# Performance work log

Hardware: AMD Instinct MI355X
Metric: run time of the kernel (lower is better)

The kernel has to match this reference:

```python
import jax, jax.numpy as jnp
import numpy as np

CLAMP_MIN, CLAMP_MAX = 1e-7, 10.0


def _hyper_layer(H, edge_nodes, W, b, power):
    """One HyperTensorGraphConvolution forward.

    H:          [N, d] node signals
    edge_nodes: [E, k] int node indices per hyperedge (k-1 < num_sample, so
                the sampling branch of the original code never triggers and the
                aggregation is the full power-mean over the k-1 neighbors)
    """
    H = jnp.clip(H, CLAMP_MIN, CLAMP_MAX)          # torch.clamp_(H, ...)
    inv_p = 1.0 / power
    Hp = H ** power                                 # [N, d]
    gathered = Hp[edge_nodes]                       # [E, k, d]
    edge_sum = gathered.sum(axis=1, keepdims=True)  # [E, 1, d]
    k = edge_nodes.shape[1]
    # power-mean of the other (k-1) nodes in the hyperedge, per incidence
    contrib = ((edge_sum - gathered) / (k - 1)) ** inv_p   # [E, k, d]
    # new_signal = H.clone(); scatter-add contributions per (edge, node)
    d = H.shape[1]
    new_signal = H.at[edge_nodes.reshape(-1)].add(contrib.reshape(-1, d))
    # row-normalize (rowsum^-1, inf -> 0)
    rowsum = new_signal.sum(axis=1, keepdims=True)
    r_inv = jnp.where(rowsum != 0, 1.0 / rowsum, 0.0)
    AH = new_signal * r_inv
    return AH @ W + b


def setup_inputs() -> dict:
    key = jax.random.key(0)
    k_x, k_e, k_w1, k_b1, k_w2, k_b2 = jax.random.split(key, 6)
    N, d, E, k, c = 100000, 128, 25000, 32, 40
    x = jax.random.uniform(k_x, (N, d), dtype=jnp.float32)
    edge_nodes = jax.random.randint(k_e, (E, k), 0, N, dtype=jnp.int64)
    std1 = 1.0 / np.sqrt(16.0)
    W1 = jax.random.uniform(k_w1, (d, 16), jnp.float32, -std1, std1)
    b1 = jax.random.uniform(k_b1, (16,), jnp.float32, -std1, std1)
    std2 = 1.0 / np.sqrt(float(c))
    W2 = jax.random.uniform(k_w2, (16, c), jnp.float32, -std2, std2)
    b2 = jax.random.uniform(k_b2, (c,), jnp.float32, -std2, std2)
    return {"x": x, "edge_nodes": edge_nodes, "W1": W1, "b1": b1,
            "W2": W2, "b2": b2, "power": 2}


def reference(x, edge_nodes, W1, b1, W2, b2, power):
    H = jax.nn.relu(_hyper_layer(x, edge_nodes, W1, b1, float(power)))
    # dropout is identity at inference
    out = _hyper_layer(H, edge_nodes, W2, b2, float(power))
    return out
```

## Files before the change

### kernel.cpp

```cpp
#include <hip/hip_runtime.h>
#include <hip/hip_fp16.h>
#include <math.h>

#define CAP 64
#define D1 128
#define D2 16
#define C_OUT 40
#define K_EDGE 32
#define CLAMP_LO 1e-7f
#define CLAMP_HI 10.0f
#define SQRT_INV31 0.1796053020267749f

typedef unsigned short ushort_t;

__global__ __launch_bounds__(256) void k_setup(const float* __restrict__ x,
                                               __half2* __restrict__ Hp,
                                               const int* __restrict__ idx,
                                               int* __restrict__ deg,
                                               ushort_t* __restrict__ lst,
                                               const float* __restrict__ W1,
                                               float* __restrict__ W1t,
                                               __half2* __restrict__ S,
                                               float* __restrict__ S2,
                                               int n4, int total, int E) {
    int i = blockIdx.x * 256 + threadIdx.x;
    if (i < n4) {
        float4 v = ((const float4*)x)[i];
        v.x = fminf(fmaxf(v.x, CLAMP_LO), CLAMP_HI);
        v.y = fminf(fmaxf(v.y, CLAMP_LO), CLAMP_HI);
        v.z = fminf(fmaxf(v.z, CLAMP_LO), CLAMP_HI);
        v.w = fminf(fmaxf(v.w, CLAMP_LO), CLAMP_HI);
        Hp[2 * i]     = __floats2half2_rn(v.x * v.x, v.y * v.y);
        Hp[2 * i + 1] = __floats2half2_rn(v.z * v.z, v.w * v.w);
    }
    if (i < total) {
        int n = idx[i];
        int e = i >> 5;
        int pos = atomicAdd(&deg[n], 1);
        if (pos < CAP) lst[n * CAP + pos] = (ushort_t)e;
    }
    if (i < D1 * D2) W1t[(i & 15) * D1 + (i >> 4)] = W1[i];
    if (i < 64) S[(size_t)E * 64 + i] = __floats2half2_rn(0.0f, 0.0f);
    if (i < D2) S2[(size_t)E * D2 + i] = 0.0f;
}

__global__ __launch_bounds__(256) void k_edge_sum(const __half2* __restrict__ Hp,
                                                  const int* __restrict__ idx,
                                                  __half2* __restrict__ S, int E) {
    int w = threadIdx.x >> 6;
    int lane = threadIdx.x & 63;
    int eA = blockIdx.x * 8 + w * 2;
    int nid = idx[eA * K_EDGE + lane];
    float a0 = 0.0f, a1 = 0.0f, b0 = 0.0f, b1 = 0.0f;
#pragma unroll
    for (int j = 0; j < K_EDGE; j++) {
        int nA = __builtin_amdgcn_readlane(nid, j);
        int nB = __builtin_amdgcn_readlane(nid, 32 + j);
        __half2 hA = Hp[(size_t)nA * 64 + lane];
        __half2 hB = Hp[(size_t)nB * 64 + lane];
        a0 += __low2float(hA); a1 += __high2float(hA);
        b0 += __low2float(hB); b1 += __high2float(hB);
    }
    S[(size_t)eA * 64 + lane]       = __floats2half2_rn(a0, a1);
    S[(size_t)(eA + 1) * 64 + lane] = __floats2half2_rn(b0, b1);
}

__global__ __launch_bounds__(256) void k_node1(const __half2* __restrict__ Hp,
                                               const __half2* __restrict__ S,
                                               const int* __restrict__ deg,
                                               const ushort_t* __restrict__ lst,
                                               const float* __restrict__ W1t,
                                               const float* __restrict__ b1,
                                               float* __restrict__ Hp2, int N, int E) {
    int w = threadIdx.x >> 6;
    int lane = threadIdx.x & 63;
    int pair = blockIdx.x * 4 + w;
    int n0 = pair * 2, n1 = n0 + 1;
    int c = lane & 15, j = lane >> 4;

    int2 dg2 = ((const int2*)deg)[pair];
    int dg0 = min(dg2.x, CAP), dg1 = min(dg2.y, CAP);
    int sl = lane & 15;
    int nodesel = (lane < 16) ? n0 : n1;
    ushort_t idu = (lane < 32) ? lst[nodesel * CAP + sl] : (ushort_t)0;
    int dsel = (lane < 16) ? dg0 : dg1;
    int e_sel = (lane < 32 && sl < dsel) ? (int)idu : E;

    __half2 hph0 = Hp[(size_t)n0 * 64 + lane];
    __half2 hph1 = Hp[(size_t)n1 * 64 + lane];

    __half2 sv0[16], sv1[16];
#pragma unroll
    for (int t = 0; t < 16; t++) {
        int e = __builtin_amdgcn_readlane(e_sel, t);
        sv0[t] = S[(size_t)e * 64 + lane];
    }
#pragma unroll
    for (int t = 0; t < 16; t++) {
        int e = __builtin_amdgcn_readlane(e_sel, 16 + t);
        sv1[t] = S[(size_t)e * 64 + lane];
    }

    float hp00 = __low2float(hph0), hp01 = __high2float(hph0);
    float hp10 = __low2float(hph1), hp11 = __high2float(hph1);

    float a00 = 0.0f, a01 = 0.0f, a10 = 0.0f, a11 = 0.0f;
#pragma unroll
    for (int t = 0; t < 16; t++) {
        a00 += __builtin_amdgcn_sqrtf(fmaxf(__low2float(sv0[t])  - hp00, 0.0f));
        a01 += __builtin_amdgcn_sqrtf(fmaxf(__high2float(sv0[t]) - hp01, 0.0f));
    }
#pragma unroll
    for (int t = 0; t < 16; t++) {
        a10 += __builtin_amdgcn_sqrtf(fmaxf(__low2float(sv1[t])  - hp10, 0.0f));
        a11 += __builtin_amdgcn_sqrtf(fmaxf(__high2float(sv1[t]) - hp11, 0.0f));
    }
    for (int t = 16; t < dg0; t++) {
        int e = lst[n0 * CAP + t];
        __half2 sh = S[(size_t)e * 64 + lane];
        a00 += __builtin_amdgcn_sqrtf(fmaxf(__low2float(sh)  - hp00, 0.0f));
        a01 += __builtin_amdgcn_sqrtf(fmaxf(__high2float(sh) - hp01, 0.0f));
    }
    for (int t = 16; t < dg1; t++) {
        int e = lst[n1 * CAP + t];
        __half2 sh = S[(size_t)e * 64 + lane];
        a10 += __builtin_amdgcn_sqrtf(fmaxf(__low2float(sh)  - hp10, 0.0f));
        a11 += __builtin_amdgcn_sqrtf(fmaxf(__high2float(sh) - hp11, 0.0f));
    }

    float ns00 = __builtin_amdgcn_sqrtf(hp00) + a00 * SQRT_INV31;
    float ns01 = __builtin_amdgcn_sqrtf(hp01) + a01 * SQRT_INV31;
    float ns10 = __builtin_amdgcn_sqrtf(hp10) + a10 * SQRT_INV31;
    float ns11 = __builtin_amdgcn_sqrtf(hp11) + a11 * SQRT_INV31;

    __shared__ float AHs[4][2][D1];
    AHs[w][0][2 * lane]     = ns00;
    AHs[w][0][2 * lane + 1] = ns01;
    AHs[w][1][2 * lane]     = ns10;
    AHs[w][1][2 * lane + 1] = ns11;

    float v0 = ns00 + ns01, v1 = ns10 + ns11;
#pragma unroll
    for (int m = 1; m < 64; m <<= 1) {
        v0 += __shfl_xor(v0, m, 64);
        v1 += __shfl_xor(v1, m, 64);
    }
    float r0 = __builtin_amdgcn_rcpf(v0);
    float r1 = __builtin_amdgcn_rcpf(v1);

    __threadfence_block();

    const float4* a0p = (const float4*)(&AHs[w][0][j * 32]);
    const float4* a1p = (const float4*)(&AHs[w][1][j * 32]);
    const float4* w1p = (const float4*)(W1t + c * D1 + j * 32);
    float p0 = 0.0f, p1 = 0.0f;
#pragma unroll
    for (int tt = 0; tt < 8; tt++) {
        float4 wv = w1p[tt];
        float4 x0 = a0p[tt];
        float4 x1 = a1p[tt];
        p0 += x0.x * wv.x + x0.y * wv.y + x0.z * wv.z + x0.w * wv.w;
        p1 += x1.x * wv.x + x1.y * wv.y + x1.z * wv.z + x1.w * wv.w;
    }
    p0 += __shfl_xor(p0, 16, 64);
    p0 += __shfl_xor(p0, 32, 64);
    p1 += __shfl_xor(p1, 16, 64);
    p1 += __shfl_xor(p1, 32, 64);
    if (lane < D2) {
        float bb = b1[c];
        float o0 = bb + p0 * r0;
        float o1 = bb + p1 * r1;
        float cl0 = fminf(fmaxf(o0, CLAMP_LO), CLAMP_HI);
        float cl1 = fminf(fmaxf(o1, CLAMP_LO), CLAMP_HI);
        Hp2[(size_t)n0 * D2 + c] = cl0 * cl0;
        Hp2[(size_t)n1 * D2 + c] = cl1 * cl1;
    }
}

__global__ __launch_bounds__(256) void k_edge_sum2(const float* __restrict__ Hp2,
                                                   const int* __restrict__ idx,
                                                   float* __restrict__ S2, int E) {
    int e = blockIdx.x * 16 + (threadIdx.x >> 4);
    int col = threadIdx.x & 15;
    if (e >= E) return;
    float acc = 0.0f;
#pragma unroll
    for (int j = 0; j < K_EDGE; j++) {
        int n = idx[e * K_EDGE + j];
        acc += Hp2[(size_t)n * D2 + col];
    }
    S2[(size_t)e * D2 + col] = acc;
}

__global__ __launch_bounds__(256) void k_node2(const float* __restrict__ Hp2,
                                               const float* __restrict__ S2,
                                               const int* __restrict__ deg,
                                               const ushort_t* __restrict__ lst,
                                               const float* __restrict__ W2,
                                               const float* __restrict__ b2,
                                               float* __restrict__ out, int N, int E) {
    int w = threadIdx.x >> 6;
    int lane = threadIdx.x & 63;
    int pair = blockIdx.x * 4 + w;
    int n0 = pair * 2, n1 = n0 + 1;
    int col = lane & 15;
    int node = lane >> 5;
    int gg = (lane >> 4) & 1;
    int nn = node ? n1 : n0;

    int2 dg2 = ((const int2*)deg)[pair];
    int dg0 = min(dg2.x, CAP), dg1 = min(dg2.y, CAP);
    int sl = lane & 15;
    ushort_t idu = (lane < 32) ? lst[((lane < 16) ? n0 : n1) * CAP + sl] : (ushort_t)0;
    int dsel = (lane < 16) ? dg0 : dg1;
    int e_sel = (lane < 32 && sl < dsel) ? (int)idu : E;

    float hp = Hp2[(size_t)nn * D2 + col];
    int dgn = node ? dg1 : dg0;

    int ev[8];
#pragma unroll
    for (int t = 0; t < 8; t++) ev[t] = __shfl(e_sel, node * 16 + 2 * t + gg, 64);
    float sv[8];
#pragma unroll
    for (int t = 0; t < 8; t++) sv[t] = S2[(size_t)ev[t] * D2 + col];

    float acc = 0.0f;
#pragma unroll
    for (int t = 0; t < 8; t++)
        acc += __builtin_amdgcn_sqrtf(fmaxf(sv[t] - hp, 0.0f));
    for (int t = 16; t < dgn; t++) {
        int e = lst[nn * CAP + t];
        float s = S2[(size_t)e * D2 + col];
        if (gg == 0) acc += __builtin_amdgcn_sqrtf(fmaxf(s - hp, 0.0f));
    }
    acc += __shfl_xor(acc, 16, 64);
    float ns = __builtin_amdgcn_sqrtf(hp) + acc * SQRT_INV31;

    float v = ns;
#pragma unroll
    for (int m = 1; m < 16; m <<= 1) v += __shfl_xor(v, m, 64);
    float r = __builtin_amdgcn_rcpf(v);

    __shared__ float AHs[4][2][D2];
    if (gg == 0) AHs[w][node][col] = ns * r;
    __threadfence_block();

    if (lane < C_OUT) {
        float o0 = b2[lane], o1 = o0;
#pragma unroll
        for (int i = 0; i < D2; i++) {
            float wv = W2[i * C_OUT + lane];
            o0 += AHs[w][0][i] * wv;
            o1 += AHs[w][1][i] * wv;
        }
        out[(size_t)n0 * C_OUT + lane] = o0;
        out[(size_t)n1 * C_OUT + lane] = o1;
    }
}

extern "C" void kernel_launch(void* const* d_in, const int* in_sizes, int n_in,
                              void* d_out, int out_size, void* d_ws, size_t ws_size,
                              hipStream_t stream) {
    const float* x   = (const float*)d_in[0];
    const int*   idx = (const int*)d_in[1];
    const float* W1  = (const float*)d_in[2];
    const float* b1  = (const float*)d_in[3];
    const float* W2  = (const float*)d_in[4];
    const float* b2  = (const float*)d_in[5];
    float* out = (float*)d_out;

    int N = in_sizes[0] / D1;
    int E = in_sizes[1] / K_EDGE;

    __half2* Hp = (__half2*)d_ws;
    __half2* S  = Hp + (size_t)N * 64;
    float* Hp2  = (float*)(S + (size_t)(E + 1) * 64);
    float* S2   = Hp2 + (size_t)N * D2;
    float* W1t  = S2 + (size_t)(E + 1) * D2;
    int*   deg  = (int*)(W1t + D1 * D2);
    ushort_t* lst = (ushort_t*)(deg + N);

    int total = E * K_EDGE;
    int n4 = N * D1 / 4;

    (void)hipMemsetAsync(deg, 0, (size_t)N * sizeof(int), stream);
    k_setup<<<(n4 + 255) / 256, 256, 0, stream>>>(x, Hp, idx, deg, lst, W1, W1t,
                                                  S, S2, n4, total, E);
    k_edge_sum<<<E / 8, 256, 0, stream>>>(Hp, idx, S, E);
    k_node1<<<N / 8, 256, 0, stream>>>(Hp, S, deg, lst, W1t, b1, Hp2, N, E);
    k_edge_sum2<<<(E + 15) / 16, 256, 0, stream>>>(Hp2, idx, S2, E);
    k_node2<<<N / 8, 256, 0, stream>>>(Hp2, S2, deg, lst, W2, b2, out, N, E);
}
```

Baseline: 255.4 us.

## Use packed fp16 arithmetic for edge sums and node sqrt accumulation

Switches the hyperedge sums and the per-node sqrt accumulation from fp32 scalar math to packed _Float16 vector math, which halves ALU instruction count and removes the half-to-float conversions. The layer-2 node powers are stored as fp16, halving their gather traffic. k_edge_sum now processes four edges per wave and k_edge_sum2 is restructured to eight edges per wave with packed half2 loads. This risks precision loss from fp16 accumulation over 32 terms, since edge sums of values up to 100 can approach the fp16 range and sqrt in half precision is less accurate.

Measured after the change: 255.8 us. About the same (+0.2%).

```diff
diff --git a/kernel.cpp b/kernel.cpp
--- a/kernel.cpp
+++ b/kernel.cpp
@@ -12,15 +12,20 @@
 #define SQRT_INV31 0.1796053020267749f
 
 typedef unsigned short ushort_t;
+typedef _Float16 hv2 __attribute__((ext_vector_type(2)));
+
+__device__ __forceinline__ hv2 hv2_zero() {
+    hv2 z; z.x = (_Float16)0; z.y = (_Float16)0; return z;
+}
 
 __global__ __launch_bounds__(256) void k_setup(const float* __restrict__ x,
-                                               __half2* __restrict__ Hp,
+                                               hv2* __restrict__ Hp,
                                                const int* __restrict__ idx,
                                                int* __restrict__ deg,
                                                ushort_t* __restrict__ lst,
                                                const float* __restrict__ W1,
                                                float* __restrict__ W1t,
-                                               __half2* __restrict__ S,
+                                               hv2* __restrict__ S,
                                                float* __restrict__ S2,
                                                int n4, int total, int E) {
     int i = blockIdx.x * 256 + threadIdx.x;
@@ -30,8 +35,9 @@
         v.y = fminf(fmaxf(v.y, CLAMP_LO), CLAMP_HI);
         v.z = fminf(fmaxf(v.z, CLAMP_LO), CLAMP_HI);
         v.w = fminf(fmaxf(v.w, CLAMP_LO), CLAMP_HI);
-        Hp[2 * i]     = __floats2half2_rn(v.x * v.x, v.y * v.y);
-        Hp[2 * i + 1] = __floats2half2_rn(v.z * v.z, v.w * v.w);
+        hv2 h0; h0.x = (_Float16)(v.x * v.x); h0.y = (_Float16)(v.y * v.y);
+        hv2 h1; h1.x = (_Float16)(v.z * v.z); h1.y = (_Float16)(v.w * v.w);
+        Hp[2 * i] = h0; Hp[2 * i + 1] = h1;
     }
     if (i < total) {
         int n = idx[i];
@@ -40,38 +46,46 @@
         if (pos < CAP) lst[n * CAP + pos] = (ushort_t)e;
     }
     if (i < D1 * D2) W1t[(i & 15) * D1 + (i >> 4)] = W1[i];
-    if (i < 64) S[(size_t)E * 64 + i] = __floats2half2_rn(0.0f, 0.0f);
+    if (i < 64) S[(size_t)E * 64 + i] = hv2_zero();
     if (i < D2) S2[(size_t)E * D2 + i] = 0.0f;
 }
 
-__global__ __launch_bounds__(256) void k_edge_sum(const __half2* __restrict__ Hp,
+__global__ __launch_bounds__(256) void k_edge_sum(const hv2* __restrict__ Hp,
                                                   const int* __restrict__ idx,
-                                                  __half2* __restrict__ S, int E) {
+                                                  hv2* __restrict__ S, int E) {
     int w = threadIdx.x >> 6;
     int lane = threadIdx.x & 63;
-    int eA = blockIdx.x * 8 + w * 2;
-    int nid = idx[eA * K_EDGE + lane];
-    float a0 = 0.0f, a1 = 0.0f, b0 = 0.0f, b1 = 0.0f;
+    int eA = (blockIdx.x * 4 + w) * 4;
+    if (eA + 4 > E) eA = E - 4;
+    int nid0 = idx[eA * K_EDGE + lane];
+    int nid1 = idx[eA * K_EDGE + 64 + lane];
+    hv2 acc[4][2];
+#pragma unroll
+    for (int k = 0; k < 4; k++) { acc[k][0] = hv2_zero(); acc[k][1] = hv2_zero(); }
 #pragma unroll
     for (int j = 0; j < K_EDGE; j++) {
-        int nA = __builtin_amdgcn_readlane(nid, j);
-        int nB = __builtin_amdgcn_readlane(nid, 32 + j);
-        __half2 hA = Hp[(size_t)nA * 64 + lane];
-        __half2 hB = Hp[(size_t)nB * 64 + lane];
-        a0 += __low2float(hA); a1 += __high2float(hA);
-        b0 += __low2float(hB); b1 += __high2float(hB);
-    }
-    S[(size_t)eA * 64 + lane]       = __floats2half2_rn(a0, a1);
-    S[(size_t)(eA + 1) * 64 + lane] = __floats2half2_rn(b0, b1);
-}
-
-__global__ __launch_bounds__(256) void k_node1(const __half2* __restrict__ Hp,
-                                               const __half2* __restrict__ S,
+        int g = j >> 4;
+        int nA = __builtin_amdgcn_readlane(nid0, j);
+        int nB = __builtin_amdgcn_readlane(nid0, 32 + j);
+        int nC = __builtin_amdgcn_readlane(nid1, j);
+        int nD = __builtin_amdgcn_readlane(nid1, 32 + j);
+        acc[0][g] += Hp[(size_t)nA * 64 + lane];
+        acc[1][g] += Hp[(size_t)nB * 64 + lane];
+        acc[2][g] += Hp[(size_t)nC * 64 + lane];
+        acc[3][g] += Hp[(size_t)nD * 64 + lane];
+    }
+#pragma unroll
+    for (int k = 0; k < 4; k++)
+        S[(size_t)(eA + k) * 64 + lane] = acc[k][0] + acc[k][1];
+}
+
+__global__ __launch_bounds__(256) void k_node1(const hv2* __restrict__ Hp,
+                                               const hv2* __restrict__ S,
                                                const int* __restrict__ deg,
                                                const ushort_t* __restrict__ lst,
                                                const float* __restrict__ W1t,
                                                const float* __restrict__ b1,
-                                               float* __restrict__ Hp2, int N, int E) {
+                                               _Float16* __restrict__ Hp2, int N, int E) {
     int w = threadIdx.x >> 6;
     int lane = threadIdx.x & 63;
     int pair = blockIdx.x * 4 + w;
@@ -86,10 +100,10 @@
     int dsel = (lane < 16) ? dg0 : dg1;
     int e_sel = (lane < 32 && sl < dsel) ? (int)idu : E;
 
-    __half2 hph0 = Hp[(size_t)n0 * 64 + lane];
-    __half2 hph1 = Hp[(size_t)n1 * 64 + lane];
-
-    __half2 sv0[16], sv1[16];
+    hv2 hph0 = Hp[(size_t)n0 * 64 + lane];
+    hv2 hph1 = Hp[(size_t)n1 * 64 + lane];
+
+    hv2 sv0[16], sv1[16];
 #pragma unroll
     for (int t = 0; t < 16; t++) {
         int e = __builtin_amdgcn_readlane(e_sel, t);
@@ -101,37 +115,38 @@
         sv1[t] = S[(size_t)e * 64 + lane];
     }
 
-    float hp00 = __low2float(hph0), hp01 = __high2float(hph0);
-    float hp10 = __low2float(hph1), hp11 = __high2float(hph1);
-
-    float a00 = 0.0f, a01 = 0.0f, a10 = 0.0f, a11 = 0.0f;
-#pragma unroll
-    for (int t = 0; t < 16; t++) {
-        a00 += __builtin_amdgcn_sqrtf(fmaxf(__low2float(sv0[t])  - hp00, 0.0f));
-        a01 += __builtin_amdgcn_sqrtf(fmaxf(__high2float(sv0[t]) - hp01, 0.0f));
-    }
-#pragma unroll
-    for (int t = 0; t < 16; t++) {
-        a10 += __builtin_amdgcn_sqrtf(fmaxf(__low2float(sv1[t])  - hp10, 0.0f));
-        a11 += __builtin_amdgcn_sqrtf(fmaxf(__high2float(sv1[t]) - hp11, 0.0f));
+    hv2 z = hv2_zero();
+    hv2 A0a = z, A0b = z, A1a = z, A1b = z;
+#pragma unroll
+    for (int t = 0; t < 16; t += 2) {
+        hv2 d0 = __builtin_elementwise_max(sv0[t] - hph0, z);
+        hv2 d1 = __builtin_elementwise_max(sv0[t + 1] - hph0, z);
+        A0a += __builtin_elementwise_sqrt(d0);
+        A0b += __builtin_elementwise_sqrt(d1);
+    }
+#pragma unroll
+    for (int t = 0; t < 16; t += 2) {
+        hv2 d0 = __builtin_elementwise_max(sv1[t] - hph1, z);
+        hv2 d1 = __builtin_elementwise_max(sv1[t + 1] - hph1, z);
+        A1a += __builtin_elementwise_sqrt(d0);
+        A1b += __builtin_elementwise_sqrt(d1);
     }
     for (int t = 16; t < dg0; t++) {
         int e = lst[n0 * CAP + t];
-        __half2 sh = S[(size_t)e * 64 + lane];
-        a00 += __builtin_amdgcn_sqrtf(fmaxf(__low2float(sh)  - hp00, 0.0f));
-        a01 += __builtin_amdgcn_sqrtf(fmaxf(__high2float(sh) - hp01, 0.0f));
+        hv2 d = __builtin_elementwise_max(S[(size_t)e * 64 + lane] - hph0, z);
+        A0a += __builtin_elementwise_sqrt(d);
     }
     for (int t = 16; t < dg1; t++) {
         int e = lst[n1 * CAP + t];
-        __half2 sh = S[(size_t)e * 64 + lane];
-        a10 += __builtin_amdgcn_sqrtf(fmaxf(__low2float(sh)  - hp10, 0.0f));
-        a11 += __builtin_amdgcn_sqrtf(fmaxf(__high2float(sh) - hp11, 0.0f));
-    }
-
-    float ns00 = __builtin_amdgcn_sqrtf(hp00) + a00 * SQRT_INV31;
-    float ns01 = __builtin_amdgcn_sqrtf(hp01) + a01 * SQRT_INV31;
-    float ns10 = __builtin_amdgcn_sqrtf(hp10) + a10 * SQRT_INV31;
-    float ns11 = __builtin_amdgcn_sqrtf(hp11) + a11 * SQRT_INV31;
+        hv2 d = __builtin_elementwise_max(S[(size_t)e * 64 + lane] - hph1, z);
+        A1a += __builtin_elementwise_sqrt(d);
+    }
+    hv2 A0 = A0a + A0b, A1 = A1a + A1b;
+
+    float ns00 = __builtin_amdgcn_sqrtf((float)hph0.x) + (float)A0.x * SQRT_INV31;
+    float ns01 = __builtin_amdgcn_sqrtf((float)hph0.y) + (float)A0.y * SQRT_INV31;
+    float ns10 = __builtin_amdgcn_sqrtf((float)hph1.x) + (float)A1.x * SQRT_INV31;
+    float ns11 = __builtin_amdgcn_sqrtf((float)hph1.y) + (float)A1.y * SQRT_INV31;
 
     __shared__ float AHs[4][2][D1];
     AHs[w][0][2 * lane]     = ns00;
@@ -172,27 +187,31 @@
         float o1 = bb + p1 * r1;
         float cl0 = fminf(fmaxf(o0, CLAMP_LO), CLAMP_HI);
         float cl1 = fminf(fmaxf(o1, CLAMP_LO), CLAMP_HI);
-        Hp2[(size_t)n0 * D2 + c] = cl0 * cl0;
-        Hp2[(size_t)n1 * D2 + c] = cl1 * cl1;
-    }
-}
-
-__global__ __launch_bounds__(256) void k_edge_sum2(const float* __restrict__ Hp2,
+        Hp2[(size_t)n0 * D2 + c] = (_Float16)(cl0 * cl0);
+        Hp2[(size_t)n1 * D2 + c] = (_Float16)(cl1 * cl1);
+    }
+}
+
+__global__ __launch_bounds__(256) void k_edge_sum2(const hv2* __restrict__ Hp2v,
                                                    const int* __restrict__ idx,
-                                                   float* __restrict__ S2, int E) {
-    int e = blockIdx.x * 16 + (threadIdx.x >> 4);
-    int col = threadIdx.x & 15;
-    if (e >= E) return;
-    float acc = 0.0f;
-#pragma unroll
-    for (int j = 0; j < K_EDGE; j++) {
-        int n = idx[e * K_EDGE + j];
-        acc += Hp2[(size_t)n * D2 + col];
-    }
-    S2[(size_t)e * D2 + col] = acc;
-}
-
-__global__ __launch_bounds__(256) void k_node2(const float* __restrict__ Hp2,
+                                                   float2* __restrict__ S2v, int E) {
+    int w = threadIdx.x >> 6;
+    int lane = threadIdx.x & 63;
+    int sub = lane >> 3;
+    int cp = lane & 7;
+    int e = (blockIdx.x * 4 + w) * 8 + sub;
+    if (e >= E) e = E - 1;
+    const int* ip = idx + (size_t)e * K_EDGE;
+    hv2 g0 = hv2_zero(), g1 = hv2_zero();
+#pragma unroll
+    for (int j = 0; j < 16; j++)  g0 += Hp2v[(size_t)ip[j] * 8 + cp];
+#pragma unroll
+    for (int j = 16; j < 32; j++) g1 += Hp2v[(size_t)ip[j] * 8 + cp];
+    float2 s; s.x = (float)g0.x + (float)g1.x; s.y = (float)g0.y + (float)g1.y;
+    S2v[(size_t)e * 8 + cp] = s;
+}
+
+__global__ __launch_bounds__(256) void k_node2(const _Float16* __restrict__ Hp2,
                                                const float* __restrict__ S2,
                                                const int* __restrict__ deg,
                                                const ushort_t* __restrict__ lst,
@@ -215,7 +234,7 @@
     int dsel = (lane < 16) ? dg0 : dg1;
     int e_sel = (lane < 32 && sl < dsel) ? (int)idu : E;
 
-    float hp = Hp2[(size_t)nn * D2 + col];
+    float hp = (float)Hp2[(size_t)nn * D2 + col];
     int dgn = node ? dg1 : dg0;
 
     int ev[8];
@@ -273,10 +292,10 @@
     int N = in_sizes[0] / D1;
     int E = in_sizes[1] / K_EDGE;
 
-    __half2* Hp = (__half2*)d_ws;
-    __half2* S  = Hp + (size_t)N * 64;
-    float* Hp2  = (float*)(S + (size_t)(E + 1) * 64);
-    float* S2   = Hp2 + (size_t)N * D2;
+    hv2* Hp = (hv2*)d_ws;
+    hv2* S  = Hp + (size_t)N * 64;
+    _Float16* Hp2h = (_Float16*)(S + (size_t)(E + 1) * 64);
+    float* S2   = (float*)(Hp2h + (size_t)N * D2);
     float* W1t  = S2 + (size_t)(E + 1) * D2;
     int*   deg  = (int*)(W1t + D1 * D2);
     ushort_t* lst = (ushort_t*)(deg + N);
@@ -287,8 +306,8 @@
     (void)hipMemsetAsync(deg, 0, (size_t)N * sizeof(int), stream);
     k_setup<<<(n4 + 255) / 256, 256, 0, stream>>>(x, Hp, idx, deg, lst, W1, W1t,
                                                   S, S2, n4, total, E);
-    k_edge_sum<<<E / 8, 256, 0, stream>>>(Hp, idx, S, E);
-    k_node1<<<N / 8, 256, 0, stream>>>(Hp, S, deg, lst, W1t, b1, Hp2, N, E);
-    k_edge_sum2<<<(E + 15) / 16, 256, 0, stream>>>(Hp2, idx, S2, E);
-    k_node2<<<N / 8, 256, 0, stream>>>(Hp2, S2, deg, lst, W2, b2, out, N, E);
-}
+    k_edge_sum<<<(E + 15) / 16, 256, 0, stream>>>(Hp, idx, S, E);
+    k_node1<<<N / 8, 256, 0, stream>>>(Hp, S, deg, lst, W1t, b1, Hp2h, N, E);
+    k_edge_sum2<<<(E + 31) / 32, 256, 0, stream>>>((const hv2*)Hp2h, idx, (float2*)S2, E);
+    k_node2<<<N / 8, 256, 0, stream>>>(Hp2h, S2, deg, lst, W2, b2, out, N, E);
+}
```
